# Kernel optimization log

Hardware: AMD Instinct MI355X
Metric: run time of the kernel (lower is better)

The kernel has to match this reference:

```python
import jax, jax.numpy as jnp
import numpy as np

B = 16384          # batch
F = 256            # num_features
H1, H2 = 32, 16    # hidden_units


def setup_inputs() -> dict:
    key = jax.random.key(0)
    ks = jax.random.split(key, 7)
    return {
        "x":  jax.random.normal(ks[0], (B, F), dtype=jnp.float32),
        "W1": jax.random.normal(ks[1], (F, 1, H1), dtype=jnp.float32) * 0.5,
        "b1": jax.random.normal(ks[2], (F, H1), dtype=jnp.float32) * 0.1,
        "W2": jax.random.normal(ks[3], (F, H1, H2), dtype=jnp.float32) * (1.0 / np.sqrt(H1)),
        "b2": jax.random.normal(ks[4], (F, H2), dtype=jnp.float32) * 0.1,
        "W3": jax.random.normal(ks[5], (F, H2, 1), dtype=jnp.float32) * (1.0 / np.sqrt(H2)),
        "b3": jax.random.normal(ks[6], (F, 1), dtype=jnp.float32) * 0.1,
    }


def reference(x, W1, b1, W2, b2, W3, b3):
    # Per-feature tiny MLP 1->H1->H2->1, batched over features as grouped GEMMs.
    # x: [B, F] (each feature is a scalar input to its own network)
    h1 = jax.nn.relu(jnp.einsum('bf,fh->bfh', x, W1[:, 0, :]) + b1)          # [B,F,H1]
    h2 = jax.nn.relu(jnp.einsum('bfh,fhk->bfk', h1, W2) + b2)                 # [B,F,H2]
    contrib = jnp.einsum('bfk,fk->bf', h2, W3[:, :, 0]) + b3[:, 0]           # [B,F]
    out = jnp.sum(contrib, axis=1, keepdims=True)                             # [B,1]
    return jax.nn.sigmoid(out)
```

## Files before the change

### kernel.cpp

```cpp
#include <hip/hip_runtime.h>
#include <math.h>

#define B_TOTAL 16384
#define F_TOTAL 256
#define H1 32
#define H2 16
#define FPB 32
#define RPB 128

typedef _Float16 f16;
typedef __attribute__((ext_vector_type(2))) _Float16 f16x2;
typedef __attribute__((ext_vector_type(8))) _Float16 f16x8;
typedef __attribute__((ext_vector_type(4))) float floatx4;

union F8 { uint4 u; f16x2 h2[4]; f16x8 h8; };

__global__ __launch_bounds__(64) void nam_pack(
    const float* __restrict__ W1, const float* __restrict__ b1,
    const float* __restrict__ W2, const float* __restrict__ b2,
    const float* __restrict__ W3,
    uint4* __restrict__ pkB,
    uint4* __restrict__ pkW,
    float2* __restrict__ pkE)
{
    const int f = blockIdx.x;
    const int lane = threadIdx.x;
    const int n = lane & 15, q = lane >> 4;

    F8 H, L;
    #pragma unroll
    for (int j = 0; j < 8; ++j) {
        float w = W2[(size_t)f * (H1 * H2) + (q * 8 + j) * H2 + n];
        f16 hi = (f16)w;
        H.h8[j] = hi;
        L.h8[j] = (f16)(w - (float)hi);
    }
    pkB[(size_t)f * 128 + lane] = H.u;
    pkB[(size_t)f * 128 + 64 + lane] = L.u;

    if (n == 0) {
        F8 A, Bb;
        #pragma unroll
        for (int j = 0; j < 8; ++j) {
            A.h8[j]  = (f16)W1[(size_t)f * H1 + q * 8 + j];
            Bb.h8[j] = (f16)b1[(size_t)f * H1 + q * 8 + j];
        }
        pkW[((size_t)f * 4 + q) * 2]     = A.u;
        pkW[((size_t)f * 4 + q) * 2 + 1] = Bb.u;
    }
    if (q == 0) {
        float2 e;
        e.x = b2[(size_t)f * H2 + n];
        e.y = W3[(size_t)f * H2 + n];
        pkE[(size_t)f * 16 + n] = e;
    }
}

__global__ __launch_bounds__(256, 4) void nam_main(
    const float* __restrict__ x,
    const float* __restrict__ b3,
    const uint4* __restrict__ pkB,
    const uint4* __restrict__ pkW,
    const float2* __restrict__ pkE,
    float* __restrict__ part)
{
    __shared__ float  xs[FPB][RPB];
    __shared__ uint4  w1b1s[FPB * 4 * 2];
    __shared__ float2 b2w3s[FPB * 16];
    __shared__ float  b3s[FPB];

    const int t = threadIdx.x;
    const int lane = t & 63;
    const int wave = t >> 6;
    const int n = lane & 15, q = lane >> 4;
    const int b0 = blockIdx.x * RPB;
    const int f0 = blockIdx.y * FPB;

    {
        int r = t >> 1, c0 = (t & 1) * 16;
        const float4* xrow = (const float4*)(x + (size_t)(b0 + r) * F_TOTAL + f0 + c0);
        #pragma unroll
        for (int i = 0; i < 4; ++i) {
            float4 v = xrow[i];
            xs[c0 + i * 4 + 0][r] = v.x; xs[c0 + i * 4 + 1][r] = v.y;
            xs[c0 + i * 4 + 2][r] = v.z; xs[c0 + i * 4 + 3][r] = v.w;
        }
    }
    w1b1s[t] = pkW[(size_t)f0 * 8 + t];
    ((uint4*)b2w3s)[t] = ((const uint4*)pkE)[(size_t)f0 * 8 + t];
    if (t < FPB) b3s[t] = b3[f0 + t];
    __syncthreads();

    const uint4* pB = pkB + (size_t)f0 * 128 + lane;
    uint4 bh[2], bl[2];
    bh[0] = pB[0];   bl[0] = pB[64];
    bh[1] = pB[128]; bl[1] = pB[192];

    floatx4 acc1 = {0.f, 0.f, 0.f, 0.f};
    floatx4 acc2 = {0.f, 0.f, 0.f, 0.f};
    const int rb = wave * 32;
    const f16x2 z2 = {(f16)0, (f16)0};

    #pragma unroll 2
    for (int fi = 0; fi < FPB; ++fi) {
        F8 Bh, Bl;
        Bh.u = bh[fi & 1];
        Bl.u = bl[fi & 1];
        int nf = (fi + 2 < FPB) ? fi + 2 : fi;
        bh[fi & 1] = pB[(size_t)nf * 128];
        bl[fi & 1] = pB[(size_t)nf * 128 + 64];

        const float xm1 = xs[fi][rb + n];
        const float xm2 = xs[fi][rb + 16 + n];
        F8 W, Bi;
        W.u  = w1b1s[(fi * 4 + q) * 2];
        Bi.u = w1b1s[(fi * 4 + q) * 2 + 1];

        const f16 xh1 = (f16)xm1;
        const f16 xh2 = (f16)xm2;
        const f16x2 x1 = {xh1, xh1};
        const f16x2 x2 = {xh2, xh2};

        F8 A1, A2;
        #pragma unroll
        for (int tt = 0; tt < 4; ++tt) {
            f16x2 h1 = x1 * W.h2[tt] + Bi.h2[tt];
            f16x2 h2 = x2 * W.h2[tt] + Bi.h2[tt];
            A1.h2[tt] = __builtin_elementwise_max(h1, z2);
            A2.h2[tt] = __builtin_elementwise_max(h2, z2);
        }

        floatx4 c1 = {0.f, 0.f, 0.f, 0.f};
        floatx4 c2 = {0.f, 0.f, 0.f, 0.f};
        c1 = __builtin_amdgcn_mfma_f32_16x16x32_f16(A1.h8, Bh.h8, c1, 0, 0, 0);
        c1 = __builtin_amdgcn_mfma_f32_16x16x32_f16(A1.h8, Bl.h8, c1, 0, 0, 0);
        c2 = __builtin_amdgcn_mfma_f32_16x16x32_f16(A2.h8, Bh.h8, c2, 0, 0, 0);
        c2 = __builtin_amdgcn_mfma_f32_16x16x32_f16(A2.h8, Bl.h8, c2, 0, 0, 0);

        const float2 bw = b2w3s[fi * 16 + n];
        #pragma unroll
        for (int r = 0; r < 4; ++r) {
            float u1 = c1[r] + bw.x; u1 = u1 > 0.f ? u1 : 0.f;
            acc1[r] = fmaf(u1, bw.y, acc1[r]);
            float u2 = c2[r] + bw.x; u2 = u2 > 0.f ? u2 : 0.f;
            acc2[r] = fmaf(u2, bw.y, acc2[r]);
        }
    }

    float accb3 = 0.f;
    #pragma unroll
    for (int i = 0; i < FPB; ++i) accb3 += b3s[i];

    #pragma unroll
    for (int r = 0; r < 4; ++r) {
        float v1 = acc1[r], v2 = acc2[r];
        v1 += __shfl_xor(v1, 1); v2 += __shfl_xor(v2, 1);
        v1 += __shfl_xor(v1, 2); v2 += __shfl_xor(v2, 2);
        v1 += __shfl_xor(v1, 4); v2 += __shfl_xor(v2, 4);
        v1 += __shfl_xor(v1, 8); v2 += __shfl_xor(v2, 8);
        acc1[r] = v1; acc2[r] = v2;
    }
    if (n == 0) {
        float* dst = part + (size_t)blockIdx.y * B_TOTAL + b0 + rb;
        float4 o1, o2;
        o1.x = acc1[0] + accb3; o1.y = acc1[1] + accb3;
        o1.z = acc1[2] + accb3; o1.w = acc1[3] + accb3;
        o2.x = acc2[0] + accb3; o2.y = acc2[1] + accb3;
        o2.z = acc2[2] + accb3; o2.w = acc2[3] + accb3;
        *(float4*)(dst + q * 4)      = o1;
        *(float4*)(dst + 16 + q * 4) = o2;
    }
}

__global__ __launch_bounds__(256) void nam_finish(
    const float* __restrict__ part, float* __restrict__ out)
{
    const int b = blockIdx.x * 256 + threadIdx.x;
    float s = 0.f;
    #pragma unroll
    for (int g = 0; g < 8; ++g) s += part[(size_t)g * B_TOTAL + b];
    out[b] = 1.0f / (1.0f + expf(-s));
}

extern "C" void kernel_launch(void* const* d_in, const int* in_sizes, int n_in,
                              void* d_out, int out_size, void* d_ws, size_t ws_size,
                              hipStream_t stream) {
    const float* x  = (const float*)d_in[0];
    const float* W1 = (const float*)d_in[1];
    const float* b1 = (const float*)d_in[2];
    const float* W2 = (const float*)d_in[3];
    const float* b2 = (const float*)d_in[4];
    const float* W3 = (const float*)d_in[5];
    const float* b3 = (const float*)d_in[6];
    float* out = (float*)d_out;

    char* ws = (char*)d_ws;
    uint4*  pkB   = (uint4*)ws;
    uint4*  pkW   = (uint4*)(ws + (512 << 10));
    float2* pkE   = (float2*)(ws + (544 << 10));
    float*  partp = (float*)(ws + (576 << 10));

    nam_pack<<<F_TOTAL, 64, 0, stream>>>(W1, b1, W2, b2, W3, pkB, pkW, pkE);

    dim3 grid(B_TOTAL / RPB, F_TOTAL / FPB);
    nam_main<<<grid, 256, 0, stream>>>(x, b3, pkB, pkW, pkE, partp);

    nam_finish<<<B_TOTAL / 256, 256, 0, stream>>>(partp, out);
}
```

Baseline: 91.98 us.

## Retile main kernel to 16 features x 256 rows with per-feature packed weight records

Changes the block tile from 32 features x 128 rows to 16 features x 256 rows, so each wave handles 64 rows (4 MFMA tiles) and reuses each feature's weights across more rows. All per-feature weights (W2 hi/lo, W1/b1, b2/W3) are packed into one contiguous 144-uint4 record and prefetched from global into registers, replacing the LDS staging of W1/b1/b2/W3. The b3 sum is precomputed once in the pack kernel and added in the finish kernel. The trade-off is a partial-sum buffer twice as large (16 slices instead of 8) and more accumulator registers per thread.

```diff
diff --git a/kernel.cpp b/kernel.cpp
--- a/kernel.cpp
+++ b/kernel.cpp
@@ -5,8 +5,9 @@
 #define F_TOTAL 256
 #define H1 32
 #define H2 16
-#define FPB 32
-#define RPB 128
+#define FPB 16
+#define RPB 256
+#define REC 144
 
 typedef _Float16 f16;
 typedef __attribute__((ext_vector_type(2))) _Float16 f16x2;
@@ -18,14 +19,13 @@
 __global__ __launch_bounds__(64) void nam_pack(
     const float* __restrict__ W1, const float* __restrict__ b1,
     const float* __restrict__ W2, const float* __restrict__ b2,
-    const float* __restrict__ W3,
-    uint4* __restrict__ pkB,
-    uint4* __restrict__ pkW,
-    float2* __restrict__ pkE)
+    const float* __restrict__ W3, const float* __restrict__ b3,
+    uint4* __restrict__ pkR, float* __restrict__ b3sum)
 {
     const int f = blockIdx.x;
     const int lane = threadIdx.x;
     const int n = lane & 15, q = lane >> 4;
+    uint4* pF = pkR + (size_t)f * REC;
 
     F8 H, L;
     #pragma unroll
@@ -35,8 +35,8 @@
         H.h8[j] = hi;
         L.h8[j] = (f16)(w - (float)hi);
     }
-    pkB[(size_t)f * 128 + lane] = H.u;
-    pkB[(size_t)f * 128 + 64 + lane] = L.u;
+    pF[lane] = H.u;
+    pF[64 + lane] = L.u;
 
     if (n == 0) {
         F8 A, Bb;
@@ -45,29 +45,33 @@
             A.h8[j]  = (f16)W1[(size_t)f * H1 + q * 8 + j];
             Bb.h8[j] = (f16)b1[(size_t)f * H1 + q * 8 + j];
         }
-        pkW[((size_t)f * 4 + q) * 2]     = A.u;
-        pkW[((size_t)f * 4 + q) * 2 + 1] = Bb.u;
+        pF[128 + q * 2] = A.u;
+        pF[129 + q * 2] = Bb.u;
     }
     if (q == 0) {
         float2 e;
         e.x = b2[(size_t)f * H2 + n];
         e.y = W3[(size_t)f * H2 + n];
-        pkE[(size_t)f * 16 + n] = e;
+        ((float2*)(pF + 136))[n] = e;
+    }
+    if (f == 0) {
+        float s = b3[lane] + b3[lane + 64] + b3[lane + 128] + b3[lane + 192];
+        s += __shfl_xor(s, 1);
+        s += __shfl_xor(s, 2);
+        s += __shfl_xor(s, 4);
+        s += __shfl_xor(s, 8);
+        s += __shfl_xor(s, 16);
+        s += __shfl_xor(s, 32);
+        if (lane == 0) b3sum[0] = s;
     }
 }
 
 __global__ __launch_bounds__(256, 4) void nam_main(
     const float* __restrict__ x,
-    const float* __restrict__ b3,
-    const uint4* __restrict__ pkB,
-    const uint4* __restrict__ pkW,
-    const float2* __restrict__ pkE,
+    const uint4* __restrict__ pkR,
     float* __restrict__ part)
 {
-    __shared__ float  xs[FPB][RPB];
-    __shared__ uint4  w1b1s[FPB * 4 * 2];
-    __shared__ float2 b2w3s[FPB * 16];
-    __shared__ float  b3s[FPB];
+    __shared__ float xs[FPB][RPB];
 
     const int t = threadIdx.x;
     const int lane = t & 63;
@@ -77,108 +81,106 @@
     const int f0 = blockIdx.y * FPB;
 
     {
-        int r = t >> 1, c0 = (t & 1) * 16;
-        const float4* xrow = (const float4*)(x + (size_t)(b0 + r) * F_TOTAL + f0 + c0);
+        const float4* xr = (const float4*)(x + (size_t)(b0 + t) * F_TOTAL + f0);
         #pragma unroll
         for (int i = 0; i < 4; ++i) {
-            float4 v = xrow[i];
-            xs[c0 + i * 4 + 0][r] = v.x; xs[c0 + i * 4 + 1][r] = v.y;
-            xs[c0 + i * 4 + 2][r] = v.z; xs[c0 + i * 4 + 3][r] = v.w;
-        }
-    }
-    w1b1s[t] = pkW[(size_t)f0 * 8 + t];
-    ((uint4*)b2w3s)[t] = ((const uint4*)pkE)[(size_t)f0 * 8 + t];
-    if (t < FPB) b3s[t] = b3[f0 + t];
+            float4 v = xr[i];
+            xs[i * 4 + 0][t] = v.x; xs[i * 4 + 1][t] = v.y;
+            xs[i * 4 + 2][t] = v.z; xs[i * 4 + 3][t] = v.w;
+        }
+    }
     __syncthreads();
 
-    const uint4* pB = pkB + (size_t)f0 * 128 + lane;
-    uint4 bh[2], bl[2];
-    bh[0] = pB[0];   bl[0] = pB[64];
-    bh[1] = pB[128]; bl[1] = pB[192];
-
-    floatx4 acc1 = {0.f, 0.f, 0.f, 0.f};
-    floatx4 acc2 = {0.f, 0.f, 0.f, 0.f};
-    const int rb = wave * 32;
+    const uint4* pR = pkR + (size_t)f0 * REC;
+    uint4 bh[2], bl[2], Wv[2], Bv[2];
+    float2 bwv[2];
+    #pragma unroll
+    for (int d = 0; d < 2; ++d) {
+        const uint4* pF = pR + (size_t)d * REC;
+        bh[d]  = pF[lane];
+        bl[d]  = pF[64 + lane];
+        Wv[d]  = pF[128 + q * 2];
+        Bv[d]  = pF[129 + q * 2];
+        bwv[d] = ((const float2*)(pF + 136))[n];
+    }
+
+    floatx4 acc[4] = {{0.f,0.f,0.f,0.f},{0.f,0.f,0.f,0.f},
+                      {0.f,0.f,0.f,0.f},{0.f,0.f,0.f,0.f}};
+    const int rb = wave * 64;
     const f16x2 z2 = {(f16)0, (f16)0};
 
     #pragma unroll 2
     for (int fi = 0; fi < FPB; ++fi) {
-        F8 Bh, Bl;
+        F8 Bh, Bl, W, Bi;
         Bh.u = bh[fi & 1];
         Bl.u = bl[fi & 1];
-        int nf = (fi + 2 < FPB) ? fi + 2 : fi;
-        bh[fi & 1] = pB[(size_t)nf * 128];
-        bl[fi & 1] = pB[(size_t)nf * 128 + 64];
-
-        const float xm1 = xs[fi][rb + n];
-        const float xm2 = xs[fi][rb + 16 + n];
-        F8 W, Bi;
-        W.u  = w1b1s[(fi * 4 + q) * 2];
-        Bi.u = w1b1s[(fi * 4 + q) * 2 + 1];
-
-        const f16 xh1 = (f16)xm1;
-        const f16 xh2 = (f16)xm2;
-        const f16x2 x1 = {xh1, xh1};
-        const f16x2 x2 = {xh2, xh2};
-
-        F8 A1, A2;
-        #pragma unroll
-        for (int tt = 0; tt < 4; ++tt) {
-            f16x2 h1 = x1 * W.h2[tt] + Bi.h2[tt];
-            f16x2 h2 = x2 * W.h2[tt] + Bi.h2[tt];
-            A1.h2[tt] = __builtin_elementwise_max(h1, z2);
-            A2.h2[tt] = __builtin_elementwise_max(h2, z2);
-        }
-
-        floatx4 c1 = {0.f, 0.f, 0.f, 0.f};
-        floatx4 c2 = {0.f, 0.f, 0.f, 0.f};
-        c1 = __builtin_amdgcn_mfma_f32_16x16x32_f16(A1.h8, Bh.h8, c1, 0, 0, 0);
-        c1 = __builtin_amdgcn_mfma_f32_16x16x32_f16(A1.h8, Bl.h8, c1, 0, 0, 0);
-        c2 = __builtin_amdgcn_mfma_f32_16x16x32_f16(A2.h8, Bh.h8, c2, 0, 0, 0);
-        c2 = __builtin_amdgcn_mfma_f32_16x16x32_f16(A2.h8, Bl.h8, c2, 0, 0, 0);
-
-        const float2 bw = b2w3s[fi * 16 + n];
+        W.u  = Wv[fi & 1];
+        Bi.u = Bv[fi & 1];
+        const float2 bw = bwv[fi & 1];
+
+        const int nf = (fi + 2 < FPB) ? fi + 2 : fi;
+        const uint4* pF = pR + (size_t)nf * REC;
+        bh[fi & 1]  = pF[lane];
+        bl[fi & 1]  = pF[64 + lane];
+        Wv[fi & 1]  = pF[128 + q * 2];
+        Bv[fi & 1]  = pF[129 + q * 2];
+        bwv[fi & 1] = ((const float2*)(pF + 136))[n];
+
+        #pragma unroll
+        for (int m = 0; m < 4; ++m) {
+            const float xm = xs[fi][rb + m * 16 + n];
+            const f16 xh = (f16)xm;
+            const f16x2 xp = {xh, xh};
+            F8 A;
+            #pragma unroll
+            for (int tt = 0; tt < 4; ++tt) {
+                f16x2 h = xp * W.h2[tt] + Bi.h2[tt];
+                A.h2[tt] = __builtin_elementwise_max(h, z2);
+            }
+            floatx4 c = {0.f, 0.f, 0.f, 0.f};
+            c = __builtin_amdgcn_mfma_f32_16x16x32_f16(A.h8, Bh.h8, c, 0, 0, 0);
+            c = __builtin_amdgcn_mfma_f32_16x16x32_f16(A.h8, Bl.h8, c, 0, 0, 0);
+            #pragma unroll
+            for (int r = 0; r < 4; ++r) {
+                float u = c[r] + bw.x;
+                u = u > 0.f ? u : 0.f;
+                acc[m][r] = fmaf(u, bw.y, acc[m][r]);
+            }
+        }
+    }
+
+    #pragma unroll
+    for (int m = 0; m < 4; ++m) {
         #pragma unroll
         for (int r = 0; r < 4; ++r) {
-            float u1 = c1[r] + bw.x; u1 = u1 > 0.f ? u1 : 0.f;
-            acc1[r] = fmaf(u1, bw.y, acc1[r]);
-            float u2 = c2[r] + bw.x; u2 = u2 > 0.f ? u2 : 0.f;
-            acc2[r] = fmaf(u2, bw.y, acc2[r]);
-        }
-    }
-
-    float accb3 = 0.f;
-    #pragma unroll
-    for (int i = 0; i < FPB; ++i) accb3 += b3s[i];
-
-    #pragma unroll
-    for (int r = 0; r < 4; ++r) {
-        float v1 = acc1[r], v2 = acc2[r];
-        v1 += __shfl_xor(v1, 1); v2 += __shfl_xor(v2, 1);
-        v1 += __shfl_xor(v1, 2); v2 += __shfl_xor(v2, 2);
-        v1 += __shfl_xor(v1, 4); v2 += __shfl_xor(v2, 4);
-        v1 += __shfl_xor(v1, 8); v2 += __shfl_xor(v2, 8);
-        acc1[r] = v1; acc2[r] = v2;
+            float v = acc[m][r];
+            v += __shfl_xor(v, 1);
+            v += __shfl_xor(v, 2);
+            v += __shfl_xor(v, 4);
+            v += __shfl_xor(v, 8);
+            acc[m][r] = v;
+        }
     }
     if (n == 0) {
         float* dst = part + (size_t)blockIdx.y * B_TOTAL + b0 + rb;
-        float4 o1, o2;
-        o1.x = acc1[0] + accb3; o1.y = acc1[1] + accb3;
-        o1.z = acc1[2] + accb3; o1.w = acc1[3] + accb3;
-        o2.x = acc2[0] + accb3; o2.y = acc2[1] + accb3;
-        o2.z = acc2[2] + accb3; o2.w = acc2[3] + accb3;
-        *(float4*)(dst + q * 4)      = o1;
-        *(float4*)(dst + 16 + q * 4) = o2;
+        #pragma unroll
+        for (int m = 0; m < 4; ++m) {
+            float4 o;
+            o.x = acc[m][0]; o.y = acc[m][1];
+            o.z = acc[m][2]; o.w = acc[m][3];
+            *(float4*)(dst + m * 16 + q * 4) = o;
+        }
     }
 }
 
 __global__ __launch_bounds__(256) void nam_finish(
-    const float* __restrict__ part, float* __restrict__ out)
+    const float* __restrict__ part, const float* __restrict__ b3sum,
+    float* __restrict__ out)
 {
     const int b = blockIdx.x * 256 + threadIdx.x;
-    float s = 0.f;
-    #pragma unroll
-    for (int g = 0; g < 8; ++g) s += part[(size_t)g * B_TOTAL + b];
+    float s = b3sum[0];
+    #pragma unroll
+    for (int g = 0; g < 16; ++g) s += part[(size_t)g * B_TOTAL + b];
     out[b] = 1.0f / (1.0f + expf(-s));
 }
 
@@ -195,15 +197,14 @@
     float* out = (float*)d_out;
 
     char* ws = (char*)d_ws;
-    uint4*  pkB   = (uint4*)ws;
-    uint4*  pkW   = (uint4*)(ws + (512 << 10));
-    float2* pkE   = (float2*)(ws + (544 << 10));
-    float*  partp = (float*)(ws + (576 << 10));
-
-    nam_pack<<<F_TOTAL, 64, 0, stream>>>(W1, b1, W2, b2, W3, pkB, pkW, pkE);
+    uint4* pkR   = (uint4*)ws;
+    float* b3sum = (float*)(ws + (592 << 10));
+    float* partp = (float*)(ws + (640 << 10));
+
+    nam_pack<<<F_TOTAL, 64, 0, stream>>>(W1, b1, W2, b2, W3, b3, pkR, b3sum);
 
     dim3 grid(B_TOTAL / RPB, F_TOTAL / FPB);
-    nam_main<<<grid, 256, 0, stream>>>(x, b3, pkB, pkW, pkE, partp);
-
-    nam_finish<<<B_TOTAL / 256, 256, 0, stream>>>(partp, out);
-}
+    nam_main<<<grid, 256, 0, stream>>>(x, pkR, partp);
+
+    nam_finish<<<B_TOTAL / 256, 256, 0, stream>>>(partp, b3sum, out);
+}
```

After: 92.52 us. Within noise of the previous version (+0.6%).
